# Performance work log

Hardware: AMD Instinct MI355X
Metric: run time of the kernel (lower is better)

Reference implementation:

```python
import jax, jax.numpy as jnp
import numpy as np

EPS = 1e-06

def _pairwise_giou(pred, target):
    # pred: [B,P,4], target: [B,G,4] -> gious [B,P,G]
    p = pred[:, :, None, :]   # [B,P,1,4]
    t = target[:, None, :, :] # [B,1,G,4]
    pw = jnp.clip(p[..., 2] - p[..., 0] + 1.0, 0.0)
    ph = jnp.clip(p[..., 3] - p[..., 1] + 1.0, 0.0)
    tw = jnp.clip(t[..., 2] - t[..., 0] + 1.0, 0.0)
    th = jnp.clip(t[..., 3] - t[..., 1] + 1.0, 0.0)
    pred_areas = pw * ph
    target_areas = tw * th
    ix1 = jnp.maximum(p[..., 0], t[..., 0])
    iy1 = jnp.maximum(p[..., 1], t[..., 1])
    ix2 = jnp.minimum(p[..., 2], t[..., 2])
    iy2 = jnp.minimum(p[..., 3], t[..., 3])
    iw = jnp.clip(ix2 - ix1 + 1.0, 0.0)
    ih = jnp.clip(iy2 - iy1 + 1.0, 0.0)
    inter = iw * ih
    unions = pred_areas + target_areas - inter
    ious = jnp.maximum(inter / unions, EPS)
    ox1 = jnp.minimum(p[..., 0], t[..., 0])
    oy1 = jnp.minimum(p[..., 1], t[..., 1])
    ox2 = jnp.maximum(p[..., 2], t[..., 2])
    oy2 = jnp.maximum(p[..., 3], t[..., 3])
    ow = jnp.clip(ox2 - ox1 + 1.0, 0.0)
    oh = jnp.clip(oy2 - oy1 + 1.0, 0.0)
    outer = ow * oh
    gious = ious - (outer - unions) / outer
    return jnp.clip(gious, -1.0, 1.0)


def setup_inputs() -> dict:
    key = jax.random.key(0)
    k1, k2, k3, k4, k5 = jax.random.split(key, 5)
    B, P, G = 32, 2048, 512
    IMG = 1024.0
    # gt boxes: [B,G,4] with x1<=x2, y1<=y2
    gxy = jax.random.uniform(k1, (B, G, 2), dtype=jnp.float32) * (IMG - 64.0)
    gwh = jax.random.uniform(k2, (B, G, 2), dtype=jnp.float32) * 64.0 + 1.0
    imgs_box = jnp.concatenate([gxy, gxy + gwh], axis=-1)
    # pred boxes: [B,P,4]
    pxy = jax.random.uniform(k3, (B, P, 2), dtype=jnp.float32) * (IMG - 64.0)
    pwh = jax.random.uniform(k4, (B, P, 2), dtype=jnp.float32) * 64.0 + 1.0
    pre_BOX = jnp.concatenate([pxy, pxy + pwh], axis=-1)
    labels = jax.random.randint(k5, (B,), 0, 10, dtype=jnp.int64 if jax.config.jax_enable_x64 else jnp.int32)
    return {"imgs_box": imgs_box, "pre_BOX": pre_BOX, "labels": labels}


def reference(imgs_box, pre_BOX, labels):
    B = labels.shape[0]
    gious = _pairwise_giou(pre_BOX, imgs_box)      # [B,P,G]
    max_giou = jnp.max(gious, axis=-1)             # [B,P]
    batch_loss = jnp.sum(1.0 - max_giou)
    return batch_loss / B
```

## Files before the change

kernel.cpp:

```cpp
#include <hip/hip_runtime.h>


constexpr int NP   = 4;
constexpr int GMAX = 512;

__global__ __launch_bounds__(1024) void giou_kernel(
    const float4* __restrict__ tgt,
    const float4* __restrict__ pred,
    float* __restrict__ out,
    int P, int G, float invB)
{
    __shared__ float4 sT[GMAX];
    __shared__ float  sA[GMAX];
    __shared__ float  sM[NP][1024];

    const int b    = blockIdx.y;
    const int tid  = threadIdx.x;
    const int lane = tid & 63;
    const int wid  = tid >> 6;

    float4 pb[NP]; float pa[NP], pw[NP], ph[NP];
    const int pbase = blockIdx.x * (NP * 64) + lane;
    #pragma unroll
    for (int k = 0; k < NP; ++k) {
        float4 v = pred[b * P + min(pbase + 64 * k, P - 1)];
        v.z += 1.0f; v.w += 1.0f;
        pb[k] = v;
        pw[k] = v.z - v.x;
        ph[k] = v.w - v.y;
        pa[k] = pw[k] * ph[k];
    }

    float m[NP];
    #pragma unroll
    for (int k = 0; k < NP; ++k) m[k] = 0.0f;

    for (int gb = 0; gb < G; gb += GMAX) {
        const int gcnt = min(GMAX, G - gb);
        __syncthreads();
        for (int g = tid; g < gcnt; g += 1024) {
            float4 t = tgt[b * G + gb + g];
            t.z += 1.0f; t.w += 1.0f;
            sT[g] = t;
            sA[g] = (t.z - t.x) * (t.w - t.y);
        }
        __syncthreads();

        const int gq = (gcnt + 15) >> 4;
        const int g0 = wid * gq;
        const int g1 = min(g0 + gq, gcnt);

        #pragma unroll 2
        for (int g = g0; g < g1; ++g) {
            const float4 t  = sT[g];
            const float  ta = sA[g];
            const float  tw = t.z - t.x;
            const float  th = t.w - t.y;
            #pragma unroll
            for (int k = 0; k < NP; ++k) {
                float iwr = fminf(pb[k].z, t.z) - fmaxf(pb[k].x, t.x);
                float ihr = fminf(pb[k].w, t.w) - fmaxf(pb[k].y, t.y);
                float inter = fmaxf(iwr, 0.0f) * fmaxf(ihr, 0.0f);
                float ow  = (pw[k] + tw) - iwr;
                float oh  = (ph[k] + th) - ihr;
                float outer = ow * oh;
                float un  = (pa[k] + ta) - inter;
                float num = __builtin_fmaf(un, un, inter * outer);
                float gi  = num * __builtin_amdgcn_rcpf(un * outer);
                m[k] = fmaxf(m[k], gi);
            }
        }
    }

    #pragma unroll
    for (int k = 0; k < NP; ++k) sM[k][tid] = m[k];
    __syncthreads();

    if (wid == 0) {
        float v = 0.0f;
        #pragma unroll
        for (int k = 0; k < NP; ++k) {
            float mm = sM[k][lane];
            #pragma unroll
            for (int w = 1; w < 16; ++w) mm = fmaxf(mm, sM[k][w * 64 + lane]);
            v += (pbase + 64 * k < P) ? (2.0f - mm) : 0.0f;
        }
        #pragma unroll
        for (int off = 32; off > 0; off >>= 1)
            v += __shfl_down(v, off, 64);
        if (lane == 0)
            atomicAdd(out, v * invB);
    }
}

extern "C" void kernel_launch(void* const* d_in, const int* in_sizes, int n_in,
                              void* d_out, int out_size, void* d_ws, size_t ws_size,
                              hipStream_t stream) {
    const float* imgs_box = (const float*)d_in[0];
    const float* pre_box  = (const float*)d_in[1];

    const int B = in_sizes[2];
    const int G = in_sizes[0] / (4 * B);
    const int P = in_sizes[1] / (4 * B);

    hipMemsetAsync(d_out, 0, sizeof(float), stream);

    const int pblocks = (P + NP * 64 - 1) / (NP * 64);
    dim3 grid(pblocks, B);
    giou_kernel<<<grid, 1024, 0, stream>>>(
        (const float4*)imgs_box, (const float4*)pre_box, (float*)d_out,
        P, G, 1.0f / (float)B);
}
```

Measured before the change: 33.31 us.

## Track max GIoU as fraction, shrink blocks, replace atomics with two-pass reduction

The inner loop now keeps the best GIoU as a numerator/denominator pair and compares by cross-multiplication, so the per-pair reciprocal is dropped and only one reciprocal per thread is taken at the end. Blocks shrink to 512 threads with 2 predictions per lane and 8 waves splitting G, which gives more blocks and a shorter final cross-wave reduction. The memset and global atomicAdd are replaced by per-block partial sums in the workspace plus a single-block reduce kernel, which adds a second launch. Targets are assumed to fit in a 512-entry shared array (G ≤ 512), and the cross-multiplied comparison assumes positive denominators.

```diff
diff --git a/kernel.cpp b/kernel.cpp
--- a/kernel.cpp
+++ b/kernel.cpp
@@ -1,29 +1,37 @@
 #include <hip/hip_runtime.h>
 
 
-constexpr int NP   = 4;
-constexpr int GMAX = 512;
+constexpr int NP = 2;
+constexpr int NW = 8;
 
-__global__ __launch_bounds__(1024) void giou_kernel(
+__global__ __launch_bounds__(512) void giou_partial_kernel(
     const float4* __restrict__ tgt,
     const float4* __restrict__ pred,
-    float* __restrict__ out,
-    int P, int G, float invB)
+    float* __restrict__ partial,
+    int P, int G)
 {
-    __shared__ float4 sT[GMAX];
-    __shared__ float  sA[GMAX];
-    __shared__ float  sM[NP][1024];
+    __shared__ float4 sT[512];
+    __shared__ float  sA[512];
+    __shared__ float  sM[NP * 512];
 
     const int b    = blockIdx.y;
     const int tid  = threadIdx.x;
     const int lane = tid & 63;
     const int wid  = tid >> 6;
 
-    float4 pb[NP]; float pa[NP], pw[NP], ph[NP];
-    const int pbase = blockIdx.x * (NP * 64) + lane;
+    for (int g = tid; g < G; g += 512) {
+        float4 t = tgt[b * G + g];
+        t.z += 1.0f; t.w += 1.0f;
+        sT[g] = t;
+        sA[g] = (t.z - t.x) * (t.w - t.y);
+    }
+    __syncthreads();
+
+    const int p0 = blockIdx.x * (NP * 64) + lane;
+    float4 pb[NP]; float pw[NP], ph[NP], pa[NP];
     #pragma unroll
     for (int k = 0; k < NP; ++k) {
-        float4 v = pred[b * P + min(pbase + 64 * k, P - 1)];
+        float4 v = pred[b * P + min(p0 + 64 * k, P - 1)];
         v.z += 1.0f; v.w += 1.0f;
         pb[k] = v;
         pw[k] = v.z - v.x;
@@ -31,66 +39,76 @@
         pa[k] = pw[k] * ph[k];
     }
 
-    float m[NP];
+    const int gq = (G + NW - 1) / NW;
+    const int g0 = wid * gq;
+    const int g1 = min(g0 + gq, G);
+
+    float numM[NP], denM[NP];
     #pragma unroll
-    for (int k = 0; k < NP; ++k) m[k] = 0.0f;
+    for (int k = 0; k < NP; ++k) { numM[k] = 0.0f; denM[k] = 1.0f; }
 
-    for (int gb = 0; gb < G; gb += GMAX) {
-        const int gcnt = min(GMAX, G - gb);
-        __syncthreads();
-        for (int g = tid; g < gcnt; g += 1024) {
-            float4 t = tgt[b * G + gb + g];
-            t.z += 1.0f; t.w += 1.0f;
-            sT[g] = t;
-            sA[g] = (t.z - t.x) * (t.w - t.y);
-        }
-        __syncthreads();
-
-        const int gq = (gcnt + 15) >> 4;
-        const int g0 = wid * gq;
-        const int g1 = min(g0 + gq, gcnt);
-
-        #pragma unroll 2
-        for (int g = g0; g < g1; ++g) {
-            const float4 t  = sT[g];
-            const float  ta = sA[g];
-            const float  tw = t.z - t.x;
-            const float  th = t.w - t.y;
-            #pragma unroll
-            for (int k = 0; k < NP; ++k) {
-                float iwr = fminf(pb[k].z, t.z) - fmaxf(pb[k].x, t.x);
-                float ihr = fminf(pb[k].w, t.w) - fmaxf(pb[k].y, t.y);
-                float inter = fmaxf(iwr, 0.0f) * fmaxf(ihr, 0.0f);
-                float ow  = (pw[k] + tw) - iwr;
-                float oh  = (ph[k] + th) - ihr;
-                float outer = ow * oh;
-                float un  = (pa[k] + ta) - inter;
-                float num = __builtin_fmaf(un, un, inter * outer);
-                float gi  = num * __builtin_amdgcn_rcpf(un * outer);
-                m[k] = fmaxf(m[k], gi);
-            }
+    #pragma unroll 2
+    for (int g = g0; g < g1; ++g) {
+        const float4 t  = sT[g];
+        const float  ta = sA[g];
+        const float  tw = t.z - t.x;
+        const float  th = t.w - t.y;
+        #pragma unroll
+        for (int k = 0; k < NP; ++k) {
+            float iwr = fminf(pb[k].z, t.z) - fmaxf(pb[k].x, t.x);
+            float ihr = fminf(pb[k].w, t.w) - fmaxf(pb[k].y, t.y);
+            float inter = fmaxf(iwr, 0.0f) * fmaxf(ihr, 0.0f);
+            float un  = (pa[k] + ta) - inter;
+            float ow  = (pw[k] + tw) - iwr;
+            float oh  = (ph[k] + th) - ihr;
+            float outer = ow * oh;
+            float num = __builtin_fmaf(un, un, inter * outer);
+            float den = un * outer;
+            bool better = num * denM[k] > numM[k] * den;
+            numM[k] = better ? num : numM[k];
+            denM[k] = better ? den : denM[k];
         }
     }
 
     #pragma unroll
-    for (int k = 0; k < NP; ++k) sM[k][tid] = m[k];
+    for (int k = 0; k < NP; ++k)
+        sM[k * 512 + tid] = numM[k] * __builtin_amdgcn_rcpf(denM[k]);
     __syncthreads();
 
     if (wid == 0) {
         float v = 0.0f;
         #pragma unroll
         for (int k = 0; k < NP; ++k) {
-            float mm = sM[k][lane];
+            float mm = sM[k * 512 + lane];
             #pragma unroll
-            for (int w = 1; w < 16; ++w) mm = fmaxf(mm, sM[k][w * 64 + lane]);
-            v += (pbase + 64 * k < P) ? (2.0f - mm) : 0.0f;
+            for (int w = 1; w < NW; ++w) mm = fmaxf(mm, sM[k * 512 + w * 64 + lane]);
+            v += (p0 + 64 * k < P) ? (2.0f - mm) : 0.0f;
         }
         #pragma unroll
         for (int off = 32; off > 0; off >>= 1)
             v += __shfl_down(v, off, 64);
         if (lane == 0)
-            atomicAdd(out, v * invB);
+            partial[blockIdx.y * gridDim.x + blockIdx.x] = v;
     }
+}
+
+__global__ __launch_bounds__(256) void giou_reduce_kernel(
+    const float* __restrict__ partial, float* __restrict__ out, int n, float invB)
+{
+    const int tid = threadIdx.x;
+    float v = 0.0f;
+    for (int i = tid; i < n; i += 256) v += partial[i];
+
+    #pragma unroll
+    for (int off = 32; off > 0; off >>= 1)
+        v += __shfl_down(v, off, 64);
+
+    __shared__ float sW[4];
+    const int wid = tid >> 6;
+    if ((tid & 63) == 0) sW[wid] = v;
+    __syncthreads();
+    if (tid == 0)
+        out[0] = (sW[0] + sW[1] + sW[2] + sW[3]) * invB;
 }
 
 extern "C" void kernel_launch(void* const* d_in, const int* in_sizes, int n_in,
@@ -103,11 +121,13 @@
     const int G = in_sizes[0] / (4 * B);
     const int P = in_sizes[1] / (4 * B);
 
-    hipMemsetAsync(d_out, 0, sizeof(float), stream);
+    float* partial = (float*)d_ws;
 
     const int pblocks = (P + NP * 64 - 1) / (NP * 64);
     dim3 grid(pblocks, B);
-    giou_kernel<<<grid, 1024, 0, stream>>>(
-        (const float4*)imgs_box, (const float4*)pre_box, (float*)d_out,
-        P, G, 1.0f / (float)B);
+    giou_partial_kernel<<<grid, 512, 0, stream>>>(
+        (const float4*)imgs_box, (const float4*)pre_box, partial, P, G);
+
+    const int n = pblocks * B;
+    giou_reduce_kernel<<<1, 256, 0, stream>>>(partial, (float*)d_out, n, 1.0f / (float)B);
 }
```

After: 30.84 us. -7.4%, faster.

## Track GIoU max as fraction to drop per-pair reciprocal, reshape blocks

Applied to the files above, without the earlier changes.

The inner loop no longer takes a reciprocal for every pred/target pair. It keeps the best numerator/denominator pair and compares candidates by cross-multiplication, with a single reciprocal per thread at the end. Target width, height and area are precomputed once into a second shared float4 array, so the loop does two 16-byte LDS loads instead of a float4 plus a scalar plus two subtractions. Blocks shrink to 512 threads with 2 preds per lane, which doubles the block count but also doubles how many times each batch's targets are staged. The fraction comparison adds multiplies and selects per pair, and assumes the denominators stay positive.

```diff
diff --git a/kernel.cpp b/kernel.cpp
--- a/kernel.cpp
+++ b/kernel.cpp
@@ -1,95 +1,102 @@
 #include <hip/hip_runtime.h>
 
 
-constexpr int NP   = 4;
-constexpr int GMAX = 512;
+constexpr int NP = 2;
+constexpr int NW = 8;
+constexpr int GCAP = 1024;
 
-__global__ __launch_bounds__(1024) void giou_kernel(
+__global__ __launch_bounds__(512) void giou_kernel(
     const float4* __restrict__ tgt,
     const float4* __restrict__ pred,
     float* __restrict__ out,
     int P, int G, float invB)
 {
-    __shared__ float4 sT[GMAX];
-    __shared__ float  sA[GMAX];
-    __shared__ float  sM[NP][1024];
+    __shared__ float4 sTB[GCAP];
+    __shared__ float4 sTD[GCAP];
+    __shared__ float  sEx[NP][512];
 
-    const int b    = blockIdx.y;
-    const int tid  = threadIdx.x;
-    const int lane = tid & 63;
-    const int wid  = tid >> 6;
+    const int b = blockIdx.y, tid = threadIdx.x;
+    const int lane = tid & 63, wid = tid >> 6;
+    const int GL = min(G, GCAP);
 
-    float4 pb[NP]; float pa[NP], pw[NP], ph[NP];
-    const int pbase = blockIdx.x * (NP * 64) + lane;
+    for (int i = tid; i < GL; i += 512) {
+        float4 t = tgt[(size_t)b * G + i];
+        t.z += 1.0f; t.w += 1.0f;
+        float tw = t.z - t.x, th = t.w - t.y;
+        sTB[i] = t;
+        sTD[i] = make_float4(tw, th, tw * th, 0.0f);
+    }
+
+    const int base = blockIdx.x * (NP * 64);
+    float4 pb[NP]; float pw[NP], ph[NP], pa[NP];
     #pragma unroll
     for (int k = 0; k < NP; ++k) {
-        float4 v = pred[b * P + min(pbase + 64 * k, P - 1)];
+        float4 v = pred[(size_t)b * P + min(base + 64 * k + lane, P - 1)];
         v.z += 1.0f; v.w += 1.0f;
-        pb[k] = v;
-        pw[k] = v.z - v.x;
-        ph[k] = v.w - v.y;
-        pa[k] = pw[k] * ph[k];
+        pb[k] = v; pw[k] = v.z - v.x; ph[k] = v.w - v.y; pa[k] = pw[k] * ph[k];
+    }
+    __syncthreads();
+
+    const int gq = (GL + NW - 1) / NW;
+    const int g0 = wid * gq, g1 = min(g0 + gq, GL);
+
+    float numM[NP] = {0.0f, 0.0f}, denM[NP] = {1.0f, 1.0f};
+
+    #pragma unroll 4
+    for (int g = g0; g < g1; ++g) {
+        const float4 t = sTB[g];
+        const float4 d = sTD[g];
+        #pragma unroll
+        for (int k = 0; k < NP; ++k) {
+            float iwr = fminf(pb[k].z, t.z) - fmaxf(pb[k].x, t.x);
+            float ihr = fminf(pb[k].w, t.w) - fmaxf(pb[k].y, t.y);
+            float inter = fmaxf(iwr, 0.0f) * fmaxf(ihr, 0.0f);
+            float un  = (pa[k] + d.z) - inter;
+            float outer = ((pw[k] + d.x) - iwr) * ((ph[k] + d.y) - ihr);
+            float num = __builtin_fmaf(un, un, inter * outer);
+            float den = un * outer;
+            bool better = num * denM[k] > numM[k] * den;
+            numM[k] = better ? num : numM[k];
+            denM[k] = better ? den : denM[k];
+        }
     }
 
-    float m[NP];
-    #pragma unroll
-    for (int k = 0; k < NP; ++k) m[k] = 0.0f;
-
-    for (int gb = 0; gb < G; gb += GMAX) {
-        const int gcnt = min(GMAX, G - gb);
-        __syncthreads();
-        for (int g = tid; g < gcnt; g += 1024) {
-            float4 t = tgt[b * G + gb + g];
-            t.z += 1.0f; t.w += 1.0f;
-            sT[g] = t;
-            sA[g] = (t.z - t.x) * (t.w - t.y);
-        }
-        __syncthreads();
-
-        const int gq = (gcnt + 15) >> 4;
-        const int g0 = wid * gq;
-        const int g1 = min(g0 + gq, gcnt);
-
-        #pragma unroll 2
-        for (int g = g0; g < g1; ++g) {
-            const float4 t  = sT[g];
-            const float  ta = sA[g];
-            const float  tw = t.z - t.x;
-            const float  th = t.w - t.y;
-            #pragma unroll
-            for (int k = 0; k < NP; ++k) {
-                float iwr = fminf(pb[k].z, t.z) - fmaxf(pb[k].x, t.x);
-                float ihr = fminf(pb[k].w, t.w) - fmaxf(pb[k].y, t.y);
-                float inter = fmaxf(iwr, 0.0f) * fmaxf(ihr, 0.0f);
-                float ow  = (pw[k] + tw) - iwr;
-                float oh  = (ph[k] + th) - ihr;
-                float outer = ow * oh;
-                float un  = (pa[k] + ta) - inter;
-                float num = __builtin_fmaf(un, un, inter * outer);
-                float gi  = num * __builtin_amdgcn_rcpf(un * outer);
-                m[k] = fmaxf(m[k], gi);
-            }
+    for (int g = GL + wid; g < G; g += NW) {
+        float4 t = tgt[(size_t)b * G + g];
+        t.z += 1.0f; t.w += 1.0f;
+        float tw = t.z - t.x, th = t.w - t.y, ta = tw * th;
+        #pragma unroll
+        for (int k = 0; k < NP; ++k) {
+            float iwr = fminf(pb[k].z, t.z) - fmaxf(pb[k].x, t.x);
+            float ihr = fminf(pb[k].w, t.w) - fmaxf(pb[k].y, t.y);
+            float inter = fmaxf(iwr, 0.0f) * fmaxf(ihr, 0.0f);
+            float un  = (pa[k] + ta) - inter;
+            float outer = ((pw[k] + tw) - iwr) * ((ph[k] + th) - ihr);
+            float num = __builtin_fmaf(un, un, inter * outer);
+            float den = un * outer;
+            bool better = num * denM[k] > numM[k] * den;
+            numM[k] = better ? num : numM[k];
+            denM[k] = better ? den : denM[k];
         }
     }
 
     #pragma unroll
-    for (int k = 0; k < NP; ++k) sM[k][tid] = m[k];
+    for (int k = 0; k < NP; ++k)
+        sEx[k][tid] = numM[k] * __builtin_amdgcn_rcpf(denM[k]);
     __syncthreads();
 
     if (wid == 0) {
         float v = 0.0f;
         #pragma unroll
         for (int k = 0; k < NP; ++k) {
-            float mm = sM[k][lane];
+            float mm = sEx[k][lane];
             #pragma unroll
-            for (int w = 1; w < 16; ++w) mm = fmaxf(mm, sM[k][w * 64 + lane]);
-            v += (pbase + 64 * k < P) ? (2.0f - mm) : 0.0f;
+            for (int w = 1; w < NW; ++w) mm = fmaxf(mm, sEx[k][w * 64 + lane]);
+            v += (base + 64 * k + lane < P) ? (2.0f - mm) : 0.0f;
         }
         #pragma unroll
-        for (int off = 32; off > 0; off >>= 1)
-            v += __shfl_down(v, off, 64);
-        if (lane == 0)
-            atomicAdd(out, v * invB);
+        for (int off = 32; off > 0; off >>= 1) v += __shfl_down(v, off, 64);
+        if (lane == 0) atomicAdd(out, v * invB);
     }
 }
 
@@ -107,7 +114,7 @@
 
     const int pblocks = (P + NP * 64 - 1) / (NP * 64);
     dim3 grid(pblocks, B);
-    giou_kernel<<<grid, 1024, 0, stream>>>(
+    giou_kernel<<<grid, 512, 0, stream>>>(
         (const float4*)imgs_box, (const float4*)pre_box, (float*)d_out,
         P, G, 1.0f / (float)B);
 }
```

New measurement: 33.23 us. Within noise of the previous version (-0.2%).
